# Kernel tuning notes

Measured on AMD Instinct MI355X. Metric: run time of the kernel, lower is better.

The kernel has to match this reference:

```python
import jax, jax.numpy as jnp
import numpy as np


def setup_inputs() -> dict:
    key = jax.random.key(0)
    k1, k2, k3 = jax.random.split(key, 3)
    N, C, W = 32, 64, 4096
    F, WW = 128, 64
    x = jax.random.normal(k1, (N, C, W), dtype=jnp.float32)
    w = jax.random.normal(k2, (F, C, WW), dtype=jnp.float32)
    b = jax.random.normal(k3, (F,), dtype=jnp.float32)
    return {"x": x, "w": w, "b": b}


def reference(x, w, b):
    # FFT-based 1D cross-correlation (the original loops over N, F, C; here batched).
    # x: [N, C, W], w: [F, C, WW], b: [F]
    N, C, W = x.shape
    F, _, WW = w.shape
    pad = 0  # module's padding kwarg
    fftsize = 1 << int(np.ceil(np.log2(W + 2 * pad + WW - 1)))  # next_power2
    out_W = W + 2 * pad - WW + 1
    # rfft of zero-padded signals and filters
    xfft = jnp.fft.rfft(x, n=fftsize, axis=-1)          # [N, C, K]
    wfft = jnp.fft.rfft(w, n=fftsize, axis=-1)          # [F, C, K]
    # cross-correlation: multiply by conj of filter spectrum, sum over channels
    offt = jnp.einsum('nck,fck->nfk', xfft, jnp.conj(wfft))  # [N, F, K]
    out = jnp.fft.irfft(offt, n=fftsize, axis=-1)[..., :out_W]  # real part, first out_W samples
    return out + b[None, :, None]
```

## Files before the change

kernel.cpp:

```cpp
#include <hip/hip_runtime.h>


#define C_TOT    64
#define F_TOT    128
#define KW       64
#define OUT_W    4033
#define W_IN     4096
#define N_BATCH  32
#define T_BLK    256
#define XROWS    320
#define XSTR     40
#define TRS      260

typedef __attribute__((ext_vector_type(8))) short  short8;
typedef __attribute__((ext_vector_type(4))) float  floatx4;

__device__ inline unsigned short f32_to_bf16(float f) {
  unsigned int u = __float_as_uint(f);
  u += 0x7FFF + ((u >> 16) & 1);
  return (unsigned short)(u >> 16);
}

__global__ __launch_bounds__(256) void conv1d_prep(
    const float* __restrict__ w, unsigned short* __restrict__ wsw) {
  int j = blockIdx.x * 256 + threadIdx.x;
  if (j < 131072) {
    int e4  = (j & 1) * 4;
    int col = (j >> 1) & 15;
    int q   = (j >> 5) & 3;
    int ft  = (j >> 7) & 3;
    int fh2 = (j >> 9) & 1;
    int tap = (j >> 10) & 1;
    int gi  = j >> 11;
    int k   = (gi & 15) + 32 * ((gi >> 4) & 1) + 16 * tap;
    int f   = fh2 * 64 + ft * 16 + col;
    int c0  = (gi >> 5) * 32 + q * 8 + e4;
    const float* src = w + ((size_t)f * C_TOT + c0) * KW + k;
    ushort4 o;
    o.x = f32_to_bf16(src[0 * KW]);
    o.y = f32_to_bf16(src[1 * KW]);
    o.z = f32_to_bf16(src[2 * KW]);
    o.w = f32_to_bf16(src[3 * KW]);
    *(ushort4*)&wsw[(size_t)j * 4] = o;
  }
}

__global__ __launch_bounds__(256, 2) void conv1d_mfma(
    const float* __restrict__ x, const unsigned short* __restrict__ wsw,
    const float* __restrict__ b, float* __restrict__ out) {
  __shared__ union SM {
    unsigned short xt[XROWS * XSTR];
    float tr[32 * TRS];
  } sm;

  const int tid  = threadIdx.x;
  const int lane = tid & 63;
  const int q    = lane >> 4;
  const int col  = lane & 15;
  const int wv   = tid >> 6;
  const int n    = blockIdx.y;
  const int t0   = blockIdx.x * T_BLK;
  const int fh2  = wv & 1;
  const int th   = wv >> 1;

  const float* xrowb = x + (size_t)n * C_TOT * W_IN;
  const short8* wp = (const short8*)wsw + fh2 * 256 + lane;

  floatx4 acc[8][4];
#pragma unroll
  for (int ms = 0; ms < 8; ++ms)
#pragma unroll
    for (int ft = 0; ft < 4; ++ft) acc[ms][ft] = (floatx4)0.0f;

#define STAGE_X(hc_)                                                           \
  {                                                                            \
    _Pragma("unroll")                                                          \
    for (int r = 0; r < 10; ++r) {                                             \
      int ti = (r % 5) * 64 + (tid & 63);                                      \
      int cl = ((r / 5) * 4 + (tid >> 6)) * 4;                                 \
      int gt = t0 + ti;                                                        \
      const float* src = xrowb + (size_t)((hc_) * 32 + cl) * W_IN + gt;        \
      float4 v = {0.f, 0.f, 0.f, 0.f};                                         \
      if (gt < W_IN) {                                                         \
        v.x = src[0];                                                          \
        v.y = src[W_IN];                                                       \
        v.z = src[2 * W_IN];                                                   \
        v.w = src[3 * W_IN];                                                   \
      }                                                                        \
      ushort4 o;                                                               \
      o.x = f32_to_bf16(v.x); o.y = f32_to_bf16(v.y);                          \
      o.z = f32_to_bf16(v.z); o.w = f32_to_bf16(v.w);                          \
      *(ushort4*)&sm.xt[ti * XSTR + cl] = o;                                   \
    }                                                                          \
  }

  STAGE_X(0)
  short8 Bt0[4];
#pragma unroll
  for (int ft = 0; ft < 4; ++ft) Bt0[ft] = wp[ft * 64];
  __syncthreads();

  for (int gi = 0; gi < 64; ++gi) {
    const int k1 = (gi & 15) + 32 * ((gi >> 4) & 1);

    short8 Bt1[4];
#pragma unroll
    for (int ft = 0; ft < 4; ++ft) Bt1[ft] = wp[512 + ft * 64];

    const unsigned short* ap = &sm.xt[(128 * th + col + k1) * XSTR + q * 8];

    short8 As[3];
    As[0] = *(const short8*)&ap[0];
    As[1] = *(const short8*)&ap[1 * 16 * XSTR];
    __builtin_amdgcn_s_setprio(1);
#pragma unroll
    for (int ms = 0; ms < 8; ++ms) {
      if (ms < 6)
        As[(ms + 2) % 3] = *(const short8*)&ap[(ms + 2) * 16 * XSTR];
#pragma unroll
      for (int ft = 0; ft < 4; ++ft)
        acc[ms][ft] = __builtin_amdgcn_mfma_f32_16x16x32_bf16(
            As[ms % 3], Bt0[ft], acc[ms][ft], 0, 0, 0);
    }
    __builtin_amdgcn_s_setprio(0);
    __builtin_amdgcn_sched_barrier(0);

    const short8* wn = (gi < 63) ? wp + 1024 : wp;
    short8 Bn[4];
#pragma unroll
    for (int ft = 0; ft < 4; ++ft) Bn[ft] = wn[ft * 64];

    short8 Az[3];
    Az[1] = *(const short8*)&ap[1 * 16 * XSTR];
    Az[2] = *(const short8*)&ap[2 * 16 * XSTR];
    __builtin_amdgcn_s_setprio(1);
#pragma unroll
    for (int ms = 0; ms < 8; ++ms) {
      if (ms < 6)
        Az[ms % 3] = *(const short8*)&ap[(ms + 3) * 16 * XSTR];
#pragma unroll
      for (int ft = 0; ft < 4; ++ft)
        acc[ms][ft] = __builtin_amdgcn_mfma_f32_16x16x32_bf16(
            Az[(ms + 1) % 3], Bt1[ft], acc[ms][ft], 0, 0, 0);
    }
    __builtin_amdgcn_s_setprio(0);

#pragma unroll
    for (int ft = 0; ft < 4; ++ft) Bt0[ft] = Bn[ft];
    wp += 1024;

    if (gi == 31) {
      __syncthreads();
      STAGE_X(1)
      __syncthreads();
    }
  }
  __syncthreads();

  const int fs_w  = fh2 * 16 + col;
  const int fs_r  = tid >> 3;
  const int seg   = tid & 7;
  const int f_r   = (fs_r >> 4) * 64 + (fs_r & 15);
  const size_t ob = ((size_t)n * F_TOT) * OUT_W;

#pragma unroll
  for (int j = 0; j < 4; ++j) {
#pragma unroll
    for (int ms = 0; ms < 8; ++ms) {
      float4 vv;
      vv.x = acc[ms][j][0];
      vv.y = acc[ms][j][1];
      vv.z = acc[ms][j][2];
      vv.w = acc[ms][j][3];
      int tl = 128 * th + 16 * ms + 4 * q;
      *(float4*)&sm.tr[fs_w * TRS + tl] = vv;
    }
    __syncthreads();
    const int f = f_r + 16 * j;
    const float bias = b[f];
    const size_t obf = ob + (size_t)f * OUT_W;
#pragma unroll
    for (int j2 = 0; j2 < 8; ++j2) {
      int tl = seg * 4 + 32 * j2;
      float4 vv = *(const float4*)&sm.tr[fs_r * TRS + tl];
      vv.x += bias; vv.y += bias; vv.z += bias; vv.w += bias;
      int t = t0 + tl;
      if (t + 3 < OUT_W) {
        *(float4*)&out[obf + t] = vv;
      } else {
        float e[4] = {vv.x, vv.y, vv.z, vv.w};
#pragma unroll
        for (int u = 0; u < 4; ++u)
          if (t + u < OUT_W) out[obf + t + u] = e[u];
      }
    }
    __syncthreads();
  }
}

extern "C" void kernel_launch(void* const* d_in, const int* in_sizes, int n_in,
                              void* d_out, int out_size, void* d_ws, size_t ws_size,
                              hipStream_t stream) {
  const float* x = (const float*)d_in[0];
  const float* w = (const float*)d_in[1];
  const float* b = (const float*)d_in[2];
  float* out = (float*)d_out;

  unsigned short* wsw = (unsigned short*)d_ws;

  conv1d_prep<<<512, 256, 0, stream>>>(w, wsw);

  dim3 grid((OUT_W + T_BLK - 1) / T_BLK, N_BATCH);
  conv1d_mfma<<<grid, 256, 0, stream>>>(x, wsw, b, out);
}
```

Measured before the change: 185.8 us.

## Merge two tap passes into one loop sharing A fragments and prefetch next operands

The two MFMA passes per iteration (taps k and k+16) are fused into a single ms loop. Each A fragment loaded from LDS now serves both taps, which cuts LDS reads roughly in half. Both B tap fragments for the next iteration, plus the first two A fragments, are prefetched in the middle of the loop, and the sched_barrier between passes is removed. This lengthens the software pipeline and should hide global and LDS latency, at the cost of more live registers, which could cause spills or lower occupancy under launch_bounds(256,2).

```diff
diff --git a/kernel.cpp b/kernel.cpp
--- a/kernel.cpp
+++ b/kernel.cpp
@@ -95,64 +95,74 @@
   }
 
   STAGE_X(0)
-  short8 Bt0[4];
-#pragma unroll
-  for (int ft = 0; ft < 4; ++ft) Bt0[ft] = wp[ft * 64];
+  short8 Bt0[4], Bt1[4];
+#pragma unroll
+  for (int ft = 0; ft < 4; ++ft) {
+    Bt0[ft] = wp[ft * 64];
+    Bt1[ft] = wp[512 + ft * 64];
+  }
   __syncthreads();
+  short8 Ac0, Ac1;
+  {
+    const unsigned short* ap0 = &sm.xt[(128 * th + col) * XSTR + q * 8];
+    Ac0 = *(const short8*)&ap0[0];
+    Ac1 = *(const short8*)&ap0[1 * 16 * XSTR];
+  }
 
   for (int gi = 0; gi < 64; ++gi) {
     const int k1 = (gi & 15) + 32 * ((gi >> 4) & 1);
-
-    short8 Bt1[4];
-#pragma unroll
-    for (int ft = 0; ft < 4; ++ft) Bt1[ft] = wp[512 + ft * 64];
-
     const unsigned short* ap = &sm.xt[(128 * th + col + k1) * XSTR + q * 8];
+    const short8* wpn = (gi < 63) ? wp + 1024 : wp;
 
     short8 As[3];
-    As[0] = *(const short8*)&ap[0];
-    As[1] = *(const short8*)&ap[1 * 16 * XSTR];
+    As[0] = Ac0;
+    As[1] = Ac1;
+    short8 Bn0[4], Bn1[4];
+
     __builtin_amdgcn_s_setprio(1);
 #pragma unroll
     for (int ms = 0; ms < 8; ++ms) {
-      if (ms < 6)
+      if (ms < 7)
         As[(ms + 2) % 3] = *(const short8*)&ap[(ms + 2) * 16 * XSTR];
+      if (ms == 5) {
+#pragma unroll
+        for (int ft = 0; ft < 4; ++ft) Bn0[ft] = wpn[ft * 64];
+      }
+      if (ms == 6) {
+#pragma unroll
+        for (int ft = 0; ft < 4; ++ft) Bn1[ft] = wpn[512 + ft * 64];
+        const int gin = (gi < 63) ? gi + 1 : 63;
+        const int k1n = (gin & 15) + 32 * ((gin >> 4) & 1);
+        const unsigned short* apn =
+            &sm.xt[(128 * th + col + k1n) * XSTR + q * 8];
+        Ac0 = *(const short8*)&apn[0];
+        Ac1 = *(const short8*)&apn[1 * 16 * XSTR];
+      }
 #pragma unroll
       for (int ft = 0; ft < 4; ++ft)
         acc[ms][ft] = __builtin_amdgcn_mfma_f32_16x16x32_bf16(
             As[ms % 3], Bt0[ft], acc[ms][ft], 0, 0, 0);
-    }
-    __builtin_amdgcn_s_setprio(0);
-    __builtin_amdgcn_sched_barrier(0);
-
-    const short8* wn = (gi < 63) ? wp + 1024 : wp;
-    short8 Bn[4];
-#pragma unroll
-    for (int ft = 0; ft < 4; ++ft) Bn[ft] = wn[ft * 64];
-
-    short8 Az[3];
-    Az[1] = *(const short8*)&ap[1 * 16 * XSTR];
-    Az[2] = *(const short8*)&ap[2 * 16 * XSTR];
-    __builtin_amdgcn_s_setprio(1);
-#pragma unroll
-    for (int ms = 0; ms < 8; ++ms) {
-      if (ms < 6)
-        Az[ms % 3] = *(const short8*)&ap[(ms + 3) * 16 * XSTR];
 #pragma unroll
       for (int ft = 0; ft < 4; ++ft)
         acc[ms][ft] = __builtin_amdgcn_mfma_f32_16x16x32_bf16(
-            Az[(ms + 1) % 3], Bt1[ft], acc[ms][ft], 0, 0, 0);
+            As[(ms + 1) % 3], Bt1[ft], acc[ms][ft], 0, 0, 0);
     }
     __builtin_amdgcn_s_setprio(0);
 
 #pragma unroll
-    for (int ft = 0; ft < 4; ++ft) Bt0[ft] = Bn[ft];
+    for (int ft = 0; ft < 4; ++ft) {
+      Bt0[ft] = Bn0[ft];
+      Bt1[ft] = Bn1[ft];
+    }
     wp += 1024;
 
     if (gi == 31) {
       __syncthreads();
       STAGE_X(1)
       __syncthreads();
+      const unsigned short* ap32 = &sm.xt[(128 * th + col) * XSTR + q * 8];
+      Ac0 = *(const short8*)&ap32[0];
+      Ac1 = *(const short8*)&ap32[1 * 16 * XSTR];
     }
   }
   __syncthreads();
```

Result: no change. 186.8 us (+0.5%).

## Split filter halves across blocks, shrinking per-wave tile for higher occupancy

Applied to the files above, without the earlier changes.

Each block now covers only one half of the filters (64), with the grid doubled along time-blocks, so every wave owns 64 time rows × 64 filters instead of 128 × 64. The accumulator array halves, and launch bounds rise to allow four blocks per CU. The software prefetch of the next weight tile is dropped in favour of loading both taps at the start of each iteration. The cost is that every x tile is staged and converted twice, once per filter half, and weight-load latency is less hidden.

```diff
diff --git a/kernel.cpp b/kernel.cpp
--- a/kernel.cpp
+++ b/kernel.cpp
@@ -45,30 +45,30 @@
   }
 }
 
-__global__ __launch_bounds__(256, 2) void conv1d_mfma(
+__global__ __launch_bounds__(256, 4) void conv1d_mfma(
     const float* __restrict__ x, const unsigned short* __restrict__ wsw,
     const float* __restrict__ b, float* __restrict__ out) {
   __shared__ union SM {
     unsigned short xt[XROWS * XSTR];
-    float tr[32 * TRS];
+    float tr[16 * TRS];
   } sm;
 
   const int tid  = threadIdx.x;
   const int lane = tid & 63;
   const int q    = lane >> 4;
   const int col  = lane & 15;
-  const int wv   = tid >> 6;
+  const int tq   = tid >> 6;
   const int n    = blockIdx.y;
-  const int t0   = blockIdx.x * T_BLK;
-  const int fh2  = wv & 1;
-  const int th   = wv >> 1;
+  const int bx   = blockIdx.x;
+  const int t0   = (bx & 15) * T_BLK;
+  const int fh   = bx >> 4;
 
   const float* xrowb = x + (size_t)n * C_TOT * W_IN;
-  const short8* wp = (const short8*)wsw + fh2 * 256 + lane;
-
-  floatx4 acc[8][4];
-#pragma unroll
-  for (int ms = 0; ms < 8; ++ms)
+  const short8* wp = (const short8*)wsw + fh * 256 + lane;
+
+  floatx4 acc[4][4];
+#pragma unroll
+  for (int ms = 0; ms < 4; ++ms)
 #pragma unroll
     for (int ft = 0; ft < 4; ++ft) acc[ms][ft] = (floatx4)0.0f;
 
@@ -95,48 +95,38 @@
   }
 
   STAGE_X(0)
-  short8 Bt0[4];
-#pragma unroll
-  for (int ft = 0; ft < 4; ++ft) Bt0[ft] = wp[ft * 64];
   __syncthreads();
 
   for (int gi = 0; gi < 64; ++gi) {
     const int k1 = (gi & 15) + 32 * ((gi >> 4) & 1);
-
-    short8 Bt1[4];
-#pragma unroll
-    for (int ft = 0; ft < 4; ++ft) Bt1[ft] = wp[512 + ft * 64];
-
-    const unsigned short* ap = &sm.xt[(128 * th + col + k1) * XSTR + q * 8];
+    const unsigned short* ap = &sm.xt[(64 * tq + col + k1) * XSTR + q * 8];
+
+    short8 Bt0[4], Bt1[4];
+#pragma unroll
+    for (int ft = 0; ft < 4; ++ft) {
+      Bt0[ft] = wp[ft * 64];
+      Bt1[ft] = wp[512 + ft * 64];
+    }
 
     short8 As[3];
     As[0] = *(const short8*)&ap[0];
     As[1] = *(const short8*)&ap[1 * 16 * XSTR];
     __builtin_amdgcn_s_setprio(1);
 #pragma unroll
-    for (int ms = 0; ms < 8; ++ms) {
-      if (ms < 6)
+    for (int ms = 0; ms < 4; ++ms) {
+      if (ms < 2)
         As[(ms + 2) % 3] = *(const short8*)&ap[(ms + 2) * 16 * XSTR];
 #pragma unroll
       for (int ft = 0; ft < 4; ++ft)
         acc[ms][ft] = __builtin_amdgcn_mfma_f32_16x16x32_bf16(
             As[ms % 3], Bt0[ft], acc[ms][ft], 0, 0, 0);
     }
-    __builtin_amdgcn_s_setprio(0);
-    __builtin_amdgcn_sched_barrier(0);
-
-    const short8* wn = (gi < 63) ? wp + 1024 : wp;
-    short8 Bn[4];
-#pragma unroll
-    for (int ft = 0; ft < 4; ++ft) Bn[ft] = wn[ft * 64];
-
     short8 Az[3];
     Az[1] = *(const short8*)&ap[1 * 16 * XSTR];
     Az[2] = *(const short8*)&ap[2 * 16 * XSTR];
-    __builtin_amdgcn_s_setprio(1);
-#pragma unroll
-    for (int ms = 0; ms < 8; ++ms) {
-      if (ms < 6)
+#pragma unroll
+    for (int ms = 0; ms < 4; ++ms) {
+      if (ms < 2)
         Az[ms % 3] = *(const short8*)&ap[(ms + 3) * 16 * XSTR];
 #pragma unroll
       for (int ft = 0; ft < 4; ++ft)
@@ -145,8 +135,6 @@
     }
     __builtin_amdgcn_s_setprio(0);
 
-#pragma unroll
-    for (int ft = 0; ft < 4; ++ft) Bt0[ft] = Bn[ft];
     wp += 1024;
 
     if (gi == 31) {
@@ -157,31 +145,29 @@
   }
   __syncthreads();
 
-  const int fs_w  = fh2 * 16 + col;
-  const int fs_r  = tid >> 3;
-  const int seg   = tid & 7;
-  const int f_r   = (fs_r >> 4) * 64 + (fs_r & 15);
+  const int fs_r  = tid >> 4;
+  const int seg   = tid & 15;
   const size_t ob = ((size_t)n * F_TOT) * OUT_W;
 
 #pragma unroll
   for (int j = 0; j < 4; ++j) {
 #pragma unroll
-    for (int ms = 0; ms < 8; ++ms) {
+    for (int ms = 0; ms < 4; ++ms) {
       float4 vv;
       vv.x = acc[ms][j][0];
       vv.y = acc[ms][j][1];
       vv.z = acc[ms][j][2];
       vv.w = acc[ms][j][3];
-      int tl = 128 * th + 16 * ms + 4 * q;
-      *(float4*)&sm.tr[fs_w * TRS + tl] = vv;
+      int tl = 64 * tq + 16 * ms + 4 * q;
+      *(float4*)&sm.tr[col * TRS + tl] = vv;
     }
     __syncthreads();
-    const int f = f_r + 16 * j;
+    const int f = fh * 64 + j * 16 + fs_r;
     const float bias = b[f];
     const size_t obf = ob + (size_t)f * OUT_W;
 #pragma unroll
-    for (int j2 = 0; j2 < 8; ++j2) {
-      int tl = seg * 4 + 32 * j2;
+    for (int j2 = 0; j2 < 4; ++j2) {
+      int tl = seg * 4 + 64 * j2;
       float4 vv = *(const float4*)&sm.tr[fs_r * TRS + tl];
       vv.x += bias; vv.y += bias; vv.z += bias; vv.w += bias;
       int t = t0 + tl;
@@ -210,6 +196,6 @@
 
   conv1d_prep<<<512, 256, 0, stream>>>(w, wsw);
 
-  dim3 grid((OUT_W + T_BLK - 1) / T_BLK, N_BATCH);
+  dim3 grid(32, N_BATCH);
   conv1d_mfma<<<grid, 256, 0, stream>>>(x, wsw, b, out);
 }
```

New measurement: 205.6 us. +10.7%, slower.
